# Kernel tuning notes

Hardware: AMD Instinct MI355X
Metric: run time of the kernel (lower is better)

## Reference

```python
import jax, jax.numpy as jnp
import numpy as np

N, E, DIN, GB, GD, LB, LD, G = 50000, 640000, 64, 128, 4, 256, 2, 1024


def setup_inputs() -> dict:
    key = jax.random.key(0)
    ks = jax.random.split(key, 20)
    p = lambda k, shape: (jax.random.normal(k, shape, dtype=jnp.float32) * 0.05)
    return {
        "x": jax.random.normal(ks[0], (N, DIN), dtype=jnp.float32),
        "edge_index": jax.random.randint(ks[1], (2, E), 0, N, dtype=jnp.int64),
        "batch": jnp.sort(jax.random.randint(ks[2], (N,), 0, G, dtype=jnp.int64)),
        "num_graphs": G,
        "W0": p(ks[3], (DIN, GB)), "b0": p(ks[4], (GB,)),
        "Wg": p(ks[5], (GD, GB, GB)), "bg": p(ks[6], (GD, GB)),
        "gamma_g": jnp.ones((GD, GB), jnp.float32), "beta_g": jnp.zeros((GD, GB), jnp.float32),
        "Wl0": p(ks[7], (GB, LB)), "bl0": p(ks[8], (LB,)),
        "Wl": p(ks[9], (LD, LB, LB)), "bl": p(ks[10], (LD, LB)),
        "gamma_l": jnp.ones((LD, LB), jnp.float32), "beta_l": jnp.zeros((LD, LB), jnp.float32),
        "Wout": p(ks[11], (LB, 2)), "bout": p(ks[12], (2,)),
    }


def reference(x, edge_index, batch, num_graphs, W0, b0, Wg, bg, gamma_g, beta_g,
              Wl0, bl0, Wl, bl, gamma_l, beta_l, Wout, bout):
    n = x.shape[0]
    src, dst = edge_index[0], edge_index[1]
    # GCN degree normalization with self loops: deg = 1 + in-degree
    deg = jax.ops.segment_sum(jnp.ones(src.shape[0], x.dtype), dst, num_segments=n) + 1.0
    dinv = jax.lax.rsqrt(deg)                 # deg^{-1/2}
    enorm = dinv[src] * dinv[dst]             # [E] edge norm
    snorm = dinv * dinv                       # [N] self-loop norm (deg^{-1})

    def gcn(h, W, b):
        hw = h @ W                                            # [N, GB]
        agg = jax.ops.segment_sum(hw[src] * enorm[:, None], dst, num_segments=n)
        return agg + hw * snorm[:, None] + b

    def bn(h, g, bt):  # training-mode batchnorm (biased var), eps=1e-5
        m = h.mean(0)
        v = h.var(0)
        return (h - m) * jax.lax.rsqrt(v + 1e-5) * g + bt

    h = jax.nn.relu(gcn(x, W0, b0))
    for i in range(Wg.shape[0]):
        h = jax.nn.relu(bn(gcn(h, Wg[i], bg[i]), gamma_g[i], beta_g[i]))
    # global_add_pool
    hp = jax.ops.segment_sum(h, batch, num_segments=num_graphs)  # [G, GB]
    h = jax.nn.relu(hp @ Wl0 + bl0)
    for i in range(Wl.shape[0]):
        h = jax.nn.relu(bn(h @ Wl[i] + bl[i], gamma_l[i], beta_l[i]))
    return h @ Wout + bout
```

## Files before the change

kernel.cpp:

```cpp
#include <hip/hip_runtime.h>

#define NN 50000
#define EE 640000
#define DINv 64
#define GBv 128
#define GDv 4
#define LBv 256
#define LDv 2
#define GGv 1024

#define NB 196
#define BCAP 4096
#define BTILE 4096
#define NBT ((EE + BTILE - 1) / BTILE)

#define NTILES ((NN + 63) / 64)

typedef _Float16 f16x8 __attribute__((ext_vector_type(8)));
typedef float f32x4 __attribute__((ext_vector_type(4)));

__device__ __forceinline__ float h2f(ushort u) {
  union { ushort u; _Float16 h; } x;
  x.u = u;
  return (float)x.h;
}
__device__ __forceinline__ ushort f2h(float f) {
  union { ushort u; _Float16 h; } x;
  x.h = (_Float16)f;
  return x.u;
}


__global__ __launch_bounds__(256) void k_bucket(const int* __restrict__ ei,
                                                int* __restrict__ bcnt,
                                                uint* __restrict__ bkt) {
  __shared__ int lcnt[NB];
  __shared__ int lbase[NB];
  __shared__ int gbase[NB];
  __shared__ int ls[256];
  __shared__ uint stage[BTILE];
  __shared__ ushort sb[BTILE];
  int tid = threadIdx.x;
  int t0 = blockIdx.x * BTILE;
  int cnt = min(BTILE, EE - t0);
  for (int i = tid; i < NB; i += 256) lcnt[i] = 0;
  __syncthreads();

  uint en[16];
  int bb[16], rk[16];
  int nper = (cnt + 255) >> 8;
  for (int k = 0; k < nper; k++) {
    int e = k * 256 + tid;
    if (e < cnt) {
      int src = ei[t0 + e];
      int dst = ei[EE + t0 + e];
      int b = dst >> 8;
      en[k] = ((uint)src << 8) | (uint)(dst & 255);
      bb[k] = b;
      rk[k] = atomicAdd(&lcnt[b], 1);
    } else {
      bb[k] = -1;
    }
  }
  __syncthreads();

  int v = (tid < NB) ? lcnt[tid] : 0;
  ls[tid] = v;
  __syncthreads();
  for (int off = 1; off < 256; off <<= 1) {
    int t = (tid >= off) ? ls[tid - off] : 0;
    __syncthreads();
    ls[tid] += t;
    __syncthreads();
  }
  if (tid < NB) {
    lbase[tid] = ls[tid] - v;
    gbase[tid] = atomicAdd(&bcnt[tid], v);
  }
  __syncthreads();

  for (int k = 0; k < nper; k++) {
    if (bb[k] >= 0) {
      int slot = lbase[bb[k]] + rk[k];
      stage[slot] = en[k];
      sb[slot] = (ushort)bb[k];
    }
  }
  __syncthreads();

  for (int i = tid; i < cnt; i += 256) {
    int b = sb[i];
    bkt[(size_t)b * BCAP + gbase[b] + (i - lbase[b])] = stage[i];
  }
}

__global__ __launch_bounds__(256) void k_bscan(const int* __restrict__ bcnt,
                                               int* __restrict__ bbase,
                                               int* __restrict__ offs) {
  __shared__ int ls[256];
  int tid = threadIdx.x;
  int v = (tid < NB) ? bcnt[tid] : 0;
  ls[tid] = v;
  __syncthreads();
  for (int off = 1; off < 256; off <<= 1) {
    int t = (tid >= off) ? ls[tid - off] : 0;
    __syncthreads();
    ls[tid] += t;
    __syncthreads();
  }
  if (tid < NB) bbase[tid] = ls[tid] - v;
  if (tid == 0) offs[NN] = EE;
}


__global__ __launch_bounds__(256) void k_csr(const uint* __restrict__ bkt,
                                             const int* __restrict__ bcnt,
                                             const int* __restrict__ bbase,
                                             int* __restrict__ offs,
                                             float* __restrict__ dinv,
                                             int* __restrict__ col) {
  __shared__ int lhist[256];
  __shared__ int lofs[256];
  __shared__ int lcur[256];
  int b = blockIdx.x;
  int cnt = bcnt[b], base = bbase[b];
  const uint* B = bkt + (size_t)b * BCAP;
  int tid = threadIdx.x;
  lhist[tid] = 0;
  __syncthreads();
  for (int i = tid; i < cnt; i += 256) atomicAdd(&lhist[B[i] & 255], 1);
  __syncthreads();
  int v = lhist[tid];
  lofs[tid] = v;
  __syncthreads();
  for (int off = 1; off < 256; off <<= 1) {
    int t = (tid >= off) ? lofs[tid - off] : 0;
    __syncthreads();
    lofs[tid] += t;
    __syncthreads();
  }
  int excl = lofs[tid] - v;
  int n = b * 256 + tid;
  if (n < NN) {
    offs[n] = base + excl;
    dinv[n] = rsqrtf((float)(v + 1));
  }
  lcur[tid] = excl;
  __syncthreads();
  for (int i = tid; i < cnt; i += 256) {
    uint e = B[i];
    int p = atomicAdd(&lcur[e & 255], 1);
    col[base + p] = (int)(e >> 8);
  }
}


__global__ void k_convW(const float* __restrict__ W0, const float* __restrict__ Wg,
                        ushort* __restrict__ Wt0, ushort* __restrict__ Wtg) {
  int idx = blockIdx.x * 256 + threadIdx.x;
  if (idx < DINv * GBv) {
    int c = idx >> 6, k = idx & 63;
    Wt0[idx] = f2h(W0[k * GBv + c]);
  } else if (idx < DINv * GBv + GDv * GBv * GBv) {
    int e = idx - DINv * GBv;
    int i = e >> 14, rem = e & 16383;
    int c = rem >> 7, k = rem & 127;
    Wtg[e] = f2h(Wg[i * GBv * GBv + k * GBv + c]);
  }
}


__global__ __launch_bounds__(256) void k_uprep(const float* __restrict__ x,
                                               const float* __restrict__ dinv,
                                               ushort* __restrict__ u) {
  int i = blockIdx.x * 256 + threadIdx.x;
  if (i >= NN * 16) return;
  int n = i >> 4;
  float4 v = ((const float4*)x)[i];
  float d = dinv[n];
  union { ushort us[4]; uint2 q; } o;
  o.us[0] = f2h(v.x * d);
  o.us[1] = f2h(v.y * d);
  o.us[2] = f2h(v.z * d);
  o.us[3] = f2h(v.w * d);
  ((uint2*)u)[i] = o.q;
}


template <int KH, int MODE>
__global__ __launch_bounds__(256) void k_agg(const ushort* __restrict__ G,
                                             const int* __restrict__ col,
                                             const int* __restrict__ offs,
                                             const float* __restrict__ dinv,
                                             const float* __restrict__ st,
                                             const float* __restrict__ gamma,
                                             const float* __restrict__ beta,
                                             ushort* __restrict__ V) {
  constexpr int VEC = KH / 16;
  __shared__ float sS[128], sT[128];
  int tid = threadIdx.x;
  if constexpr (MODE == 2) {
    if (tid < 128) {
      float mu = st[tid] * (1.f / NN);
      float var = st[128 + tid] * (1.f / NN) - mu * mu;
      float s = rsqrtf(var + 1e-5f) * gamma[tid];
      sS[tid] = s;
      sT[tid] = beta[tid] - mu * s;
    }
    __syncthreads();
  }
  int lane = tid & 63;
  int q = lane >> 4, m = lane & 15;
  int n = blockIdx.x * 16 + (tid >> 6) * 4 + q;

  float sc[VEC], tc[VEC];
  if constexpr (MODE == 2) {
#pragma unroll
    for (int v = 0; v < VEC; v++) {
      sc[v] = sS[m * VEC + v];
      tc[v] = sT[m * VEC + v];
    }
  }

  union U { uint4 v4; uint2 v2; ushort us[8]; };
  auto loadrow = [&](int s) {
    U u;
    const ushort* p = G + (long)s * KH + m * VEC;
    if constexpr (VEC == 8) u.v4 = *(const uint4*)p;
    else u.v2 = *(const uint2*)p;
    return u;
  };
  float acc[VEC];
#pragma unroll
  for (int v = 0; v < VEC; v++) acc[v] = 0.f;
  auto addrow = [&](U u, float dv) {
#pragma unroll
    for (int v = 0; v < VEC; v++) {
      float g = h2f(u.us[v]);
      if constexpr (MODE == 0) acc[v] += g;
      else if constexpr (MODE == 1) acc[v] += fmaxf(g, 0.f) * dv;
      else acc[v] += fmaxf(g * sc[v] + tc[v], 0.f) * dv;
    }
  };

  float dn = dinv[n];
  addrow(loadrow(n), dn);

  int s0 = offs[n], s1 = offs[n + 1];
  int j = s0;
  for (; j + 7 < s1; j += 8) {
    int si[8];
#pragma unroll
    for (int t = 0; t < 8; t++) si[t] = col[j + t];
    U uu[8];
#pragma unroll
    for (int t = 0; t < 8; t++) uu[t] = loadrow(si[t]);
    float dd[8];
#pragma unroll
    for (int t = 0; t < 8; t++) dd[t] = (MODE != 0) ? dinv[si[t]] : 0.f;
#pragma unroll
    for (int t = 0; t < 8; t++) addrow(uu[t], dd[t]);
  }
  for (; j + 3 < s1; j += 4) {
    int si[4];
#pragma unroll
    for (int t = 0; t < 4; t++) si[t] = col[j + t];
    U uu[4];
#pragma unroll
    for (int t = 0; t < 4; t++) uu[t] = loadrow(si[t]);
    float dd[4];
#pragma unroll
    for (int t = 0; t < 4; t++) dd[t] = (MODE != 0) ? dinv[si[t]] : 0.f;
#pragma unroll
    for (int t = 0; t < 4; t++) addrow(uu[t], dd[t]);
  }
  for (; j < s1; j++) {
    int s = col[j];
    U u = loadrow(s);
    float dv = (MODE != 0) ? dinv[s] : 0.f;
    addrow(u, dv);
  }

  U o;
#pragma unroll
  for (int v = 0; v < VEC; v++) o.us[v] = f2h(acc[v] * dn);
  ushort* op = V + (long)n * KH + m * VEC;
  if constexpr (VEC == 8) *(uint4*)op = o.v4;
  else *(uint2*)op = o.v2;
}


template <int K, bool STATS>
__global__ __launch_bounds__(256) void k_mm(const ushort* __restrict__ X,
                                            const ushort* __restrict__ Wt,
                                            const float* __restrict__ bias,
                                            float* __restrict__ stG,
                                            ushort* __restrict__ Gout) {
  constexpr int KP = K + 8;
  constexpr int CP = 136;
  constexpr bool REUSE = (K == 128);
  __shared__ __attribute__((aligned(16))) _Float16 sW[128 * KP];
  __shared__ __attribute__((aligned(16))) _Float16 sA[64 * KP];
  __shared__ __attribute__((aligned(16))) _Float16 sCbuf[REUSE ? 8 : 64 * CP];
  __shared__ float sB[128];
  __shared__ float ssum[128], ssq[128];
  _Float16* sC = REUSE ? sA : sCbuf;
  int tid = threadIdx.x;

  {
    constexpr int CH = K / 8;
    for (int i = tid; i < 128 * CH; i += 256) {
      int c = i / CH, ch = i - c * CH;
      *(uint4*)&sW[c * KP + ch * 8] = ((const uint4*)Wt)[i];
    }
  }
  if (tid < 128) {
    sB[tid] = bias[tid];
    if constexpr (STATS) {
      ssum[tid] = 0.f;
      ssq[tid] = 0.f;
    }
  }

  int w = tid >> 6, lane = tid & 63;
  int m = lane & 15, quad = lane >> 4;
  int crow = 16 * w + quad * 4;

  float ps[8], pq[8];
  if constexpr (STATS) {
#pragma unroll
    for (int ct = 0; ct < 8; ct++) { ps[ct] = 0.f; pq[ct] = 0.f; }
  }

  for (int tile = blockIdx.x; tile < NTILES; tile += gridDim.x) {
    int row0 = tile * 64;
    __syncthreads();

    {
      int r = tid >> 2, col0 = (tid & 3) * (K / 4);
      int gr = row0 + r;
      const uint4* p = (const uint4*)(X + (long)gr * K + col0);
#pragma unroll
      for (int ch = 0; ch < K / 32; ch++) {
        uint4 v = (gr < NN) ? p[ch] : make_uint4(0, 0, 0, 0);
        *(uint4*)&sA[r * KP + col0 + ch * 8] = v;
      }
    }
    __syncthreads();

    f32x4 acc[8];
#pragma unroll
    for (int ct = 0; ct < 8; ct++) acc[ct] = (f32x4){0.f, 0.f, 0.f, 0.f};
    const _Float16* pa = &sA[(16 * w + m) * KP + quad * 8];
#pragma unroll
    for (int ks = 0; ks < K; ks += 32) {
      f16x8 a = *(const f16x8*)(pa + ks);
#pragma unroll
      for (int ct = 0; ct < 8; ct++) {
        f16x8 b = *(const f16x8*)&sW[(ct * 16 + m) * KP + ks + quad * 8];
        acc[ct] = __builtin_amdgcn_mfma_f32_16x16x32_f16(a, b, acc[ct], 0, 0, 0);
      }
    }

    if constexpr (STATS) {
#pragma unroll
      for (int ct = 0; ct < 8; ct++) {
        int c = ct * 16 + m;
        float b = sB[c];
#pragma unroll
        for (int r = 0; r < 4; r++) {
          if (row0 + crow + r < NN) {
            float g = acc[ct][r] + b;
            ps[ct] += g;
            pq[ct] += g * g;
          }
        }
      }
    }
    if constexpr (REUSE) __syncthreads();

#pragma unroll
    for (int ct = 0; ct < 8; ct++) {
      int c = ct * 16 + m;
      float b = sB[c];
#pragma unroll
      for (int r = 0; r < 4; r++) sC[(crow + r) * CP + c] = (_Float16)(acc[ct][r] + b);
    }
    __syncthreads();

    {
      int r = tid >> 2, col0 = (tid & 3) * 32;
      int gr = row0 + r;
      if (gr < NN) {
        const uint4* src = (const uint4*)&sC[r * CP + col0];
        uint4* dst = (uint4*)(Gout + (long)gr * 128 + col0);
#pragma unroll
        for (int ch = 0; ch < 4; ch++) dst[ch] = src[ch];
      }
    }
  }

  if constexpr (STATS) {
#pragma unroll
    for (int ct = 0; ct < 8; ct++) {
      float s = ps[ct], q = pq[ct];
      s += __shfl_xor(s, 16);
      q += __shfl_xor(q, 16);
      s += __shfl_xor(s, 32);
      q += __shfl_xor(q, 32);
      if (quad == 0) {
        atomicAdd(&ssum[ct * 16 + m], s);
        atomicAdd(&ssq[ct * 16 + m], q);
      }
    }
    __syncthreads();
    if (tid < 128) {
      int c = (tid + blockIdx.x * 8) & 127;
      atomicAdd(&stG[c], ssum[c]);
      atomicAdd(&stG[128 + c], ssq[c]);
    }
  }
}


__global__ __launch_bounds__(128) void k_pool2(const ushort* __restrict__ G,
                                               const float* __restrict__ st,
                                               const float* __restrict__ gamma,
                                               const float* __restrict__ beta,
                                               const int* __restrict__ batch,
                                               float* __restrict__ hp) {
  __shared__ int sse[2];
  int g = blockIdx.x;
  int c = threadIdx.x;
  if (c < 2) {
    int key = g + c;
    int lo = 0, hi = NN;
    while (lo < hi) {
      int mid = (lo + hi) >> 1;
      if (batch[mid] < key) lo = mid + 1;
      else hi = mid;
    }
    sse[c] = lo;
  }
  __syncthreads();
  int s = sse[0], e = sse[1];
  float m = st[c] * (1.f / NN);
  float v = st[128 + c] * (1.f / NN) - m * m;
  float sc = rsqrtf(v + 1e-5f) * gamma[c];
  float tc = beta[c] - m * sc;
  float acc = 0.f;
  for (int n = s; n < e; n++) acc += fmaxf(h2f(G[(long)n * 128 + c]) * sc + tc, 0.f);
  hp[(long)g * 128 + c] = acc;
}


__global__ void k_colstats(const float* __restrict__ X, int rows, float* __restrict__ st) {
  int c = threadIdx.x;
  int C = blockDim.x;
  float s = 0.f, q = 0.f;
  for (int r = blockIdx.x; r < rows; r += gridDim.x) {
    float v = X[(long)r * C + c];
    s += v;
    q += v * v;
  }
  atomicAdd(&st[c], s);
  atomicAdd(&st[C + c], q);
}


template <int KIN, int MODE>
__global__ __launch_bounds__(256) void k_fc(const float* __restrict__ X,
                                            const float* __restrict__ W,
                                            const float* __restrict__ b,
                                            const float* __restrict__ st,
                                            const float* __restrict__ gamma,
                                            const float* __restrict__ beta,
                                            float* __restrict__ Y) {
  __shared__ float sx[KIN];
  int g = blockIdx.x;
  int c = threadIdx.x;
  for (int k = c; k < KIN; k += 256) {
    float v = X[(long)g * KIN + k];
    if constexpr (MODE == 2) {
      float m = st[k] * (1.f / GGv);
      float var = st[KIN + k] * (1.f / GGv) - m * m;
      v = fmaxf((v - m) * rsqrtf(var + 1e-5f) * gamma[k] + beta[k], 0.f);
    }
    sx[k] = v;
  }
  __syncthreads();
  float acc = b[c];
#pragma unroll 8
  for (int k = 0; k < KIN; k++) acc += sx[k] * W[(long)k * 256 + c];
  Y[(long)g * 256 + c] = (MODE == 0) ? fmaxf(acc, 0.f) : acc;
}

__global__ __launch_bounds__(256) void k_out(const float* __restrict__ X,
                                             const float* __restrict__ st,
                                             const float* __restrict__ gamma,
                                             const float* __restrict__ beta,
                                             const float* __restrict__ Wout,
                                             const float* __restrict__ bout,
                                             float* __restrict__ out) {
  int g = blockIdx.x * 4 + (threadIdx.x >> 6);
  int l = threadIdx.x & 63;
  float a0 = 0.f, a1 = 0.f;
  for (int k = l; k < LBv; k += 64) {
    float z = X[(long)g * LBv + k];
    float m = st[k] * (1.f / GGv);
    float var = st[LBv + k] * (1.f / GGv) - m * m;
    float x = fmaxf((z - m) * rsqrtf(var + 1e-5f) * gamma[k] + beta[k], 0.f);
    a0 += x * Wout[2 * k];
    a1 += x * Wout[2 * k + 1];
  }
  for (int off = 32; off > 0; off >>= 1) {
    a0 += __shfl_down(a0, off);
    a1 += __shfl_down(a1, off);
  }
  if (l == 0) {
    out[2 * g] = a0 + bout[0];
    out[2 * g + 1] = a1 + bout[1];
  }
}


extern "C" void kernel_launch(void* const* d_in, const int* in_sizes, int n_in,
                              void* d_out, int out_size, void* d_ws, size_t ws_size,
                              hipStream_t stream) {
  const float* x = (const float*)d_in[0];
  const int* ei = (const int*)d_in[1];
  const int* batch = (const int*)d_in[2];
  const float* W0 = (const float*)d_in[4];
  const float* b0 = (const float*)d_in[5];
  const float* Wg = (const float*)d_in[6];
  const float* bg = (const float*)d_in[7];
  const float* gamma_g = (const float*)d_in[8];
  const float* beta_g = (const float*)d_in[9];
  const float* Wl0 = (const float*)d_in[10];
  const float* bl0 = (const float*)d_in[11];
  const float* Wl = (const float*)d_in[12];
  const float* bl = (const float*)d_in[13];
  const float* gamma_l = (const float*)d_in[14];
  const float* beta_l = (const float*)d_in[15];
  const float* Wout = (const float*)d_in[16];
  const float* bout = (const float*)d_in[17];
  float* out = (float*)d_out;

  char* w = (char*)d_ws;
  auto alloc = [&](size_t bytes) {
    void* p = (void*)w;
    w += (bytes + 255) & ~(size_t)255;
    return p;
  };
  int* bcnt = (int*)alloc((size_t)NB * 4);
  float* stAll = (float*)alloc((size_t)(4 * 256 + 2 * 512) * 4);
  size_t zspan = (char*)w - (char*)bcnt;
  uint* bkt = (uint*)alloc((size_t)NB * BCAP * 4);
  int* bbase = (int*)alloc((size_t)NB * 4);
  int* offs = (int*)alloc((size_t)(NN + 1) * 4);
  int* col = (int*)alloc((size_t)EE * 4);
  float* dinv = (float*)alloc((size_t)NN * 4);
  ushort* u = (ushort*)alloc((size_t)NN * DINv * 2);
  ushort* V = (ushort*)alloc((size_t)NN * GBv * 2);
  ushort* g = (ushort*)alloc((size_t)NN * GBv * 2);
  ushort* Wt0 = (ushort*)alloc((size_t)DINv * GBv * 2);
  ushort* Wtg = (ushort*)alloc((size_t)GDv * GBv * GBv * 2);
  float* hp = (float*)alloc((size_t)GGv * GBv * 4);
  float* m1 = (float*)alloc((size_t)GGv * LBv * 4);
  float* m2 = (float*)alloc((size_t)GGv * LBv * 4);

  float* stg = stAll;
  float* sth0 = stAll + 4 * 256;
  float* sth1 = sth0 + 512;

  hipMemsetAsync(bcnt, 0, zspan, stream);

  k_bucket<<<NBT, 256, 0, stream>>>(ei, bcnt, bkt);
  k_bscan<<<1, 256, 0, stream>>>(bcnt, bbase, offs);
  k_csr<<<NB, 256, 0, stream>>>(bkt, bcnt, bbase, offs, dinv, col);
  k_convW<<<(DINv * GBv + GDv * GBv * GBv + 255) / 256, 256, 0, stream>>>(W0, Wg, Wt0, Wtg);
  k_uprep<<<(NN * 16 + 255) / 256, 256, 0, stream>>>(x, dinv, u);

  const int AGG = NN / 16;
  const int MMG = 512;

  k_agg<64, 0><<<AGG, 256, 0, stream>>>(u, col, offs, dinv, nullptr, nullptr, nullptr, V);
  k_mm<64, false><<<MMG, 256, 0, stream>>>(V, Wt0, b0, nullptr, g);

  k_agg<128, 1><<<AGG, 256, 0, stream>>>(g, col, offs, dinv, nullptr, nullptr, nullptr, V);
  k_mm<128, true><<<MMG, 256, 0, stream>>>(V, Wtg, bg, stg, g);

  for (int i = 1; i < GDv; i++) {
    k_agg<128, 2><<<AGG, 256, 0, stream>>>(g, col, offs, dinv, stg + (size_t)(i - 1) * 256,
                                           gamma_g + (size_t)(i - 1) * GBv,
                                           beta_g + (size_t)(i - 1) * GBv, V);
    k_mm<128, true><<<MMG, 256, 0, stream>>>(V, Wtg + (size_t)i * GBv * GBv,
                                             bg + (size_t)i * GBv, stg + (size_t)i * 256, g);
  }

  k_pool2<<<GGv, 128, 0, stream>>>(g, stg + 3 * 256, gamma_g + 3 * GBv, beta_g + 3 * GBv,
                                   batch, hp);

  k_fc<GBv, 0><<<GGv, 256, 0, stream>>>(hp, Wl0, bl0, nullptr, nullptr, nullptr, m1);
  k_fc<LBv, 1><<<GGv, 256, 0, stream>>>(m1, Wl, bl, nullptr, nullptr, nullptr, m2);
  k_colstats<<<256, LBv, 0, stream>>>(m2, GGv, sth0);
  k_fc<LBv, 2><<<GGv, 256, 0, stream>>>(m2, Wl + (size_t)LBv * LBv, bl + LBv, sth0,
                                        gamma_l, beta_l, m1);
  k_colstats<<<256, LBv, 0, stream>>>(m1, GGv, sth1);
  k_out<<<GGv / 4, 256, 0, stream>>>(m1, sth1, gamma_l + LBv, beta_l + LBv, Wout, bout, out);
}
```

Baseline: 451.8 us.

## Split aggregation into column-pass tiles and pad shared memory to limit occupancy

The aggregation kernel now handles a 32-column slice per pass, one block per (pass, 64-node tile), with four lanes per node each loading 8 halves. The goal is a smaller gather working set per pass, so feature-matrix columns stay in L2. It also declares a large dummy shared array, touched only behind a never-true guard, to force low occupancy, presumably to cut cache thrashing. In exchange, the edge list and dinv are re-read once per pass, and the BN scale and shift are recomputed per thread.

```diff
diff --git a/kernel.cpp b/kernel.cpp
--- a/kernel.cpp
+++ b/kernel.cpp
@@ -187,8 +187,8 @@
 }
 
 
-template <int KH, int MODE>
-__global__ __launch_bounds__(256) void k_agg(const ushort* __restrict__ G,
+template <int K, int MODE>
+__global__ __launch_bounds__(256) void k_agg(const ushort* __restrict__ Gin,
                                              const int* __restrict__ col,
                                              const int* __restrict__ offs,
                                              const float* __restrict__ dinv,
@@ -196,46 +196,49 @@
                                              const float* __restrict__ gamma,
                                              const float* __restrict__ beta,
                                              ushort* __restrict__ V) {
-  constexpr int VEC = KH / 16;
-  __shared__ float sS[128], sT[128];
+  __shared__ int pad[13312];
   int tid = threadIdx.x;
+  if (offs[NN] == -1) {
+    pad[tid] = tid;
+    __syncthreads();
+    V[pad[tid]] = 0;
+  }
+
+  int pass = blockIdx.x / NTILES;
+  int tile = blockIdx.x - pass * NTILES;
+  int row0 = tile * 64;
+  int w = tid >> 6, lane = tid & 63;
+  int gnode = lane >> 2;
+  int l4 = lane & 3;
+  int n = row0 + w * 16 + gnode;
+  int cbase = pass * 32 + l4 * 8;
+  if (n >= NN) return;
+
+  float sc[8], tc[8];
   if constexpr (MODE == 2) {
-    if (tid < 128) {
-      float mu = st[tid] * (1.f / NN);
-      float var = st[128 + tid] * (1.f / NN) - mu * mu;
-      float s = rsqrtf(var + 1e-5f) * gamma[tid];
-      sS[tid] = s;
-      sT[tid] = beta[tid] - mu * s;
-    }
-    __syncthreads();
-  }
-  int lane = tid & 63;
-  int q = lane >> 4, m = lane & 15;
-  int n = blockIdx.x * 16 + (tid >> 6) * 4 + q;
-
-  float sc[VEC], tc[VEC];
-  if constexpr (MODE == 2) {
-#pragma unroll
-    for (int v = 0; v < VEC; v++) {
-      sc[v] = sS[m * VEC + v];
-      tc[v] = sT[m * VEC + v];
-    }
-  }
-
-  union U { uint4 v4; uint2 v2; ushort us[8]; };
+#pragma unroll
+    for (int v = 0; v < 8; v++) {
+      int c = cbase + v;
+      float mu = st[c] * (1.f / NN);
+      float var = st[128 + c] * (1.f / NN) - mu * mu;
+      float s = rsqrtf(var + 1e-5f) * gamma[c];
+      sc[v] = s;
+      tc[v] = beta[c] - mu * s;
+    }
+  }
+
+  union U { uint4 v4; ushort us[8]; };
   auto loadrow = [&](int s) {
     U u;
-    const ushort* p = G + (long)s * KH + m * VEC;
-    if constexpr (VEC == 8) u.v4 = *(const uint4*)p;
-    else u.v2 = *(const uint2*)p;
+    u.v4 = *(const uint4*)(Gin + (long)s * K + cbase);
     return u;
   };
-  float acc[VEC];
-#pragma unroll
-  for (int v = 0; v < VEC; v++) acc[v] = 0.f;
+  float acc[8];
+#pragma unroll
+  for (int v = 0; v < 8; v++) acc[v] = 0.f;
   auto addrow = [&](U u, float dv) {
 #pragma unroll
-    for (int v = 0; v < VEC; v++) {
+    for (int v = 0; v < 8; v++) {
       float g = h2f(u.us[v]);
       if constexpr (MODE == 0) acc[v] += g;
       else if constexpr (MODE == 1) acc[v] += fmaxf(g, 0.f) * dv;
@@ -283,10 +286,8 @@
 
   U o;
 #pragma unroll
-  for (int v = 0; v < VEC; v++) o.us[v] = f2h(acc[v] * dn);
-  ushort* op = V + (long)n * KH + m * VEC;
-  if constexpr (VEC == 8) *(uint4*)op = o.v4;
-  else *(uint2*)op = o.v2;
+  for (int v = 0; v < 8; v++) o.us[v] = f2h(acc[v] * dn);
+  *(uint4*)(V + (long)n * K + cbase) = o.v4;
 }
 
 
@@ -581,19 +582,21 @@
   k_convW<<<(DINv * GBv + GDv * GBv * GBv + 255) / 256, 256, 0, stream>>>(W0, Wg, Wt0, Wtg);
   k_uprep<<<(NN * 16 + 255) / 256, 256, 0, stream>>>(x, dinv, u);
 
-  const int AGG = NN / 16;
   const int MMG = 512;
 
-  k_agg<64, 0><<<AGG, 256, 0, stream>>>(u, col, offs, dinv, nullptr, nullptr, nullptr, V);
+  k_agg<64, 0><<<2 * NTILES, 256, 0, stream>>>(u, col, offs, dinv, nullptr, nullptr,
+                                               nullptr, V);
   k_mm<64, false><<<MMG, 256, 0, stream>>>(V, Wt0, b0, nullptr, g);
 
-  k_agg<128, 1><<<AGG, 256, 0, stream>>>(g, col, offs, dinv, nullptr, nullptr, nullptr, V);
+  k_agg<128, 1><<<4 * NTILES, 256, 0, stream>>>(g, col, offs, dinv, nullptr, nullptr,
+                                                nullptr, V);
   k_mm<128, true><<<MMG, 256, 0, stream>>>(V, Wtg, bg, stg, g);
 
   for (int i = 1; i < GDv; i++) {
-    k_agg<128, 2><<<AGG, 256, 0, stream>>>(g, col, offs, dinv, stg + (size_t)(i - 1) * 256,
-                                           gamma_g + (size_t)(i - 1) * GBv,
-                                           beta_g + (size_t)(i - 1) * GBv, V);
+    k_agg<128, 2><<<4 * NTILES, 256, 0, stream>>>(g, col, offs, dinv,
+                                                  stg + (size_t)(i - 1) * 256,
+                                                  gamma_g + (size_t)(i - 1) * GBv,
+                                                  beta_g + (size_t)(i - 1) * GBv, V);
     k_mm<128, true><<<MMG, 256, 0, stream>>>(V, Wtg + (size_t)i * GBv * GBv,
                                              bg + (size_t)i * GBv, stg + (size_t)i * 256, g);
   }
```

After: 516.4 us. +14.3%, slower.

## Sort nodes by degree for aggregation load balance and fuse prep kernels

Applied to the files above, without the earlier changes.

Builds a degree histogram and counting-sort permutation of nodes so aggregation blocks process nodes of similar in-degree together, reducing intra-wave divergence from unequal neighbor counts. Also merges the weight conversion and input scaling kernels into one launch. Adds two small kernels (a serial scan and a permutation pass) plus an indirect perm lookup per node, and the permuted order scatters output writes.

```diff
diff --git a/kernel.cpp b/kernel.cpp
--- a/kernel.cpp
+++ b/kernel.cpp
@@ -15,6 +15,8 @@
 #define NBT ((EE + BTILE - 1) / BTILE)
 
 #define NTILES ((NN + 63) / 64)
+#define UPN (NN * 16)
+#define CONVN (DINv * GBv + GDv * GBv * GBv)
 
 typedef _Float16 f16x8 __attribute__((ext_vector_type(8)));
 typedef float f32x4 __attribute__((ext_vector_type(4)));
@@ -118,15 +120,19 @@
                                              const int* __restrict__ bbase,
                                              int* __restrict__ offs,
                                              float* __restrict__ dinv,
-                                             int* __restrict__ col) {
+                                             int* __restrict__ col,
+                                             int* __restrict__ deg,
+                                             int* __restrict__ ghist) {
   __shared__ int lhist[256];
   __shared__ int lofs[256];
   __shared__ int lcur[256];
+  __shared__ int lh2[64];
   int b = blockIdx.x;
   int cnt = bcnt[b], base = bbase[b];
   const uint* B = bkt + (size_t)b * BCAP;
   int tid = threadIdx.x;
   lhist[tid] = 0;
+  if (tid < 64) lh2[tid] = 0;
   __syncthreads();
   for (int i = tid; i < cnt; i += 256) atomicAdd(&lhist[B[i] & 255], 1);
   __syncthreads();
@@ -144,9 +150,13 @@
   if (n < NN) {
     offs[n] = base + excl;
     dinv[n] = rsqrtf((float)(v + 1));
+    int d = min(v, 63);
+    deg[n] = d;
+    atomicAdd(&lh2[d], 1);
   }
   lcur[tid] = excl;
   __syncthreads();
+  if (tid < 64 && lh2[tid]) atomicAdd(&ghist[tid], lh2[tid]);
   for (int i = tid; i < cnt; i += 256) {
     uint e = B[i];
     int p = atomicAdd(&lcur[e & 255], 1);
@@ -154,49 +164,81 @@
   }
 }
 
-
-__global__ void k_convW(const float* __restrict__ W0, const float* __restrict__ Wg,
-                        ushort* __restrict__ Wt0, ushort* __restrict__ Wtg) {
+__global__ void k_dscan(const int* __restrict__ ghist, int* __restrict__ dcur) {
+  if (threadIdx.x == 0 && blockIdx.x == 0) {
+    int run = 0;
+    for (int i = 0; i < 64; i++) {
+      dcur[i] = run;
+      run += ghist[i];
+    }
+  }
+}
+
+__global__ __launch_bounds__(256) void k_dperm(const int* __restrict__ deg,
+                                               int* __restrict__ dcur,
+                                               int* __restrict__ perm) {
+  __shared__ int lhist[64];
+  __shared__ int lbase[64];
+  int tid = threadIdx.x;
+  if (tid < 64) lhist[tid] = 0;
+  __syncthreads();
+  int n = blockIdx.x * 256 + tid;
+  int d = 0, rk = 0;
+  if (n < NN) {
+    d = deg[n];
+    rk = atomicAdd(&lhist[d], 1);
+  }
+  __syncthreads();
+  if (tid < 64 && lhist[tid]) lbase[tid] = atomicAdd(&dcur[tid], lhist[tid]);
+  __syncthreads();
+  if (n < NN) perm[lbase[d] + rk] = n;
+}
+
+
+__global__ __launch_bounds__(256) void k_prep(const float* __restrict__ x,
+                                              const float* __restrict__ dinv,
+                                              const float* __restrict__ W0,
+                                              const float* __restrict__ Wg,
+                                              ushort* __restrict__ u,
+                                              ushort* __restrict__ Wt0,
+                                              ushort* __restrict__ Wtg) {
   int idx = blockIdx.x * 256 + threadIdx.x;
-  if (idx < DINv * GBv) {
-    int c = idx >> 6, k = idx & 63;
-    Wt0[idx] = f2h(W0[k * GBv + c]);
-  } else if (idx < DINv * GBv + GDv * GBv * GBv) {
-    int e = idx - DINv * GBv;
-    int i = e >> 14, rem = e & 16383;
-    int c = rem >> 7, k = rem & 127;
-    Wtg[e] = f2h(Wg[i * GBv * GBv + k * GBv + c]);
-  }
-}
-
-
-__global__ __launch_bounds__(256) void k_uprep(const float* __restrict__ x,
-                                               const float* __restrict__ dinv,
-                                               ushort* __restrict__ u) {
-  int i = blockIdx.x * 256 + threadIdx.x;
-  if (i >= NN * 16) return;
-  int n = i >> 4;
-  float4 v = ((const float4*)x)[i];
-  float d = dinv[n];
-  union { ushort us[4]; uint2 q; } o;
-  o.us[0] = f2h(v.x * d);
-  o.us[1] = f2h(v.y * d);
-  o.us[2] = f2h(v.z * d);
-  o.us[3] = f2h(v.w * d);
-  ((uint2*)u)[i] = o.q;
-}
-
-
-template <int KH, int MODE>
-__global__ __launch_bounds__(256) void k_agg(const ushort* __restrict__ G,
+  if (idx < UPN) {
+    int n = idx >> 4;
+    float4 v = ((const float4*)x)[idx];
+    float d = dinv[n];
+    union { ushort us[4]; uint2 q; } o;
+    o.us[0] = f2h(v.x * d);
+    o.us[1] = f2h(v.y * d);
+    o.us[2] = f2h(v.z * d);
+    o.us[3] = f2h(v.w * d);
+    ((uint2*)u)[idx] = o.q;
+  } else {
+    int j = idx - UPN;
+    if (j < DINv * GBv) {
+      int c = j >> 6, k = j & 63;
+      Wt0[j] = f2h(W0[k * GBv + c]);
+    } else if (j < CONVN) {
+      int e = j - DINv * GBv;
+      int i = e >> 14, rem = e & 16383;
+      int c = rem >> 7, k = rem & 127;
+      Wtg[e] = f2h(Wg[i * GBv * GBv + k * GBv + c]);
+    }
+  }
+}
+
+
+template <int K, int MODE>
+__global__ __launch_bounds__(256) void k_agg(const ushort* __restrict__ Gin,
                                              const int* __restrict__ col,
                                              const int* __restrict__ offs,
                                              const float* __restrict__ dinv,
+                                             const int* __restrict__ perm,
                                              const float* __restrict__ st,
                                              const float* __restrict__ gamma,
                                              const float* __restrict__ beta,
                                              ushort* __restrict__ V) {
-  constexpr int VEC = KH / 16;
+  constexpr int VEC = K / 16;
   __shared__ float sS[128], sT[128];
   int tid = threadIdx.x;
   if constexpr (MODE == 2) {
@@ -211,7 +253,8 @@
   }
   int lane = tid & 63;
   int q = lane >> 4, m = lane & 15;
-  int n = blockIdx.x * 16 + (tid >> 6) * 4 + q;
+  int idx = blockIdx.x * 16 + (tid >> 6) * 4 + q;
+  int n = perm[idx];
 
   float sc[VEC], tc[VEC];
   if constexpr (MODE == 2) {
@@ -225,7 +268,7 @@
   union U { uint4 v4; uint2 v2; ushort us[8]; };
   auto loadrow = [&](int s) {
     U u;
-    const ushort* p = G + (long)s * KH + m * VEC;
+    const ushort* p = Gin + (long)s * K + m * VEC;
     if constexpr (VEC == 8) u.v4 = *(const uint4*)p;
     else u.v2 = *(const uint2*)p;
     return u;
@@ -284,7 +327,7 @@
   U o;
 #pragma unroll
   for (int v = 0; v < VEC; v++) o.us[v] = f2h(acc[v] * dn);
-  ushort* op = V + (long)n * KH + m * VEC;
+  ushort* op = V + (long)n * K + m * VEC;
   if constexpr (VEC == 8) *(uint4*)op = o.v4;
   else *(uint2*)op = o.v2;
 }
@@ -554,12 +597,16 @@
   };
   int* bcnt = (int*)alloc((size_t)NB * 4);
   float* stAll = (float*)alloc((size_t)(4 * 256 + 2 * 512) * 4);
+  int* ghist = (int*)alloc((size_t)64 * 4);
   size_t zspan = (char*)w - (char*)bcnt;
   uint* bkt = (uint*)alloc((size_t)NB * BCAP * 4);
   int* bbase = (int*)alloc((size_t)NB * 4);
   int* offs = (int*)alloc((size_t)(NN + 1) * 4);
   int* col = (int*)alloc((size_t)EE * 4);
   float* dinv = (float*)alloc((size_t)NN * 4);
+  int* deg = (int*)alloc((size_t)NN * 4);
+  int* perm = (int*)alloc((size_t)NN * 4);
+  int* dcur = (int*)alloc((size_t)64 * 4);
   ushort* u = (ushort*)alloc((size_t)NN * DINv * 2);
   ushort* V = (ushort*)alloc((size_t)NN * GBv * 2);
   ushort* g = (ushort*)alloc((size_t)NN * GBv * 2);
@@ -577,21 +624,25 @@
 
   k_bucket<<<NBT, 256, 0, stream>>>(ei, bcnt, bkt);
   k_bscan<<<1, 256, 0, stream>>>(bcnt, bbase, offs);
-  k_csr<<<NB, 256, 0, stream>>>(bkt, bcnt, bbase, offs, dinv, col);
-  k_convW<<<(DINv * GBv + GDv * GBv * GBv + 255) / 256, 256, 0, stream>>>(W0, Wg, Wt0, Wtg);
-  k_uprep<<<(NN * 16 + 255) / 256, 256, 0, stream>>>(x, dinv, u);
+  k_csr<<<NB, 256, 0, stream>>>(bkt, bcnt, bbase, offs, dinv, col, deg, ghist);
+  k_dscan<<<1, 64, 0, stream>>>(ghist, dcur);
+  k_dperm<<<NB, 256, 0, stream>>>(deg, dcur, perm);
+  k_prep<<<(UPN + CONVN + 255) / 256, 256, 0, stream>>>(x, dinv, W0, Wg, u, Wt0, Wtg);
 
   const int AGG = NN / 16;
   const int MMG = 512;
 
-  k_agg<64, 0><<<AGG, 256, 0, stream>>>(u, col, offs, dinv, nullptr, nullptr, nullptr, V);
+  k_agg<64, 0><<<AGG, 256, 0, stream>>>(u, col, offs, dinv, perm, nullptr, nullptr,
+                                        nullptr, V);
   k_mm<64, false><<<MMG, 256, 0, stream>>>(V, Wt0, b0, nullptr, g);
 
-  k_agg<128, 1><<<AGG, 256, 0, stream>>>(g, col, offs, dinv, nullptr, nullptr, nullptr, V);
+  k_agg<128, 1><<<AGG, 256, 0, stream>>>(g, col, offs, dinv, perm, nullptr, nullptr,
+                                         nullptr, V);
   k_mm<128, true><<<MMG, 256, 0, stream>>>(V, Wtg, bg, stg, g);
 
   for (int i = 1; i < GDv; i++) {
-    k_agg<128, 2><<<AGG, 256, 0, stream>>>(g, col, offs, dinv, stg + (size_t)(i - 1) * 256,
+    k_agg<128, 2><<<AGG, 256, 0, stream>>>(g, col, offs, dinv, perm,
+                                           stg + (size_t)(i - 1) * 256,
                                            gamma_g + (size_t)(i - 1) * GBv,
                                            beta_g + (size_t)(i - 1) * GBv, V);
     k_mm<128, true><<<MMG, 256, 0, stream>>>(V, Wtg + (size_t)i * GBv * GBv,
```

New measurement: 446.8 us. No clear change (-1.1%).
